# Kernel tuning notes

Hardware: AMD Instinct MI355X
Metric: run time of the kernel (lower is better)

The kernel has to match this reference:

```python
import jax, jax.numpy as jnp
import numpy as np
import math

BS, T = 256, 128
DD, DT, DB = 128, 16, 32
DH, NH, DS = 256, 4, 64
DHN = DH * NH


def _lin(key, din, dout):
    kw, kb = jax.random.split(key)
    w = jax.random.normal(kw, (din, dout), jnp.float32) * 0.02
    bb = jax.random.normal(kb, (dout,), jnp.float32) * 0.02
    return w, bb


def setup_inputs() -> dict:
    key = jax.random.key(0)
    ks = jax.random.split(key, 16)
    inp = {
        "x": jax.random.normal(ks[0], (BS, T, DD), jnp.float32),
        "a": jax.random.normal(ks[1], (BS, T, DT), jnp.float32),
        "m": jnp.ones((BS, T, DD), jnp.float32),
        "b": jax.random.normal(ks[2], (BS, DB), jnp.float32),
        "eps": jax.random.normal(ks[3], (T - 1, BS, DS), jnp.float32),
    }
    inp["bk_w"], inp["bk_b"] = _lin(ks[4], DD + DB, DH)
    inp["bv_w"], inp["bv_b"] = _lin(ks[5], DD + DB, DHN)
    inp["q_w"], inp["q_b"] = _lin(ks[6], DD + DT, DHN)
    inp["v_w"], inp["v_b"] = _lin(ks[7], DD + DT, DHN)
    inp["hk_w"], inp["hk_b"] = _lin(ks[8], DS, DH)
    inp["hv_w"], inp["hv_b"] = _lin(ks[9], DS, DHN)
    inp["mu1_w"], inp["mu1_b"] = _lin(ks[10], DHN, DS)
    inp["sg1_w"], inp["sg1_b"] = _lin(ks[11], DHN, DS)
    inp["mut_w"], inp["mut_b"] = _lin(ks[12], DHN, DS)
    inp["sgt_w"], inp["sgt_b"] = _lin(ks[13], DHN, DS)
    return inp


def reference(x, a, m, b, eps,
              bk_w, bk_b, bv_w, bv_b, q_w, q_b, v_w, v_b,
              hk_w, hk_b, hv_w, hv_b,
              mu1_w, mu1_b, sg1_w, sg1_b, mut_w, mut_b, sgt_w, sgt_b):
    bs = x.shape[0]
    inp = jnp.concatenate([x[:, 1:, :], a[:, :-1, :]], -1)   # [bs, T-1, DD+DT]
    mask = (jnp.sum(m[:, 1:, :], -1) > 0.0).astype(x.dtype)  # [bs, T-1]

    q_inp = jax.nn.relu(inp @ q_w + q_b).reshape(bs, -1, DH, NH)  # [bs,T-1,DH,NH]
    v_inp = (inp @ v_w + v_b).reshape(bs, -1, DH, NH)

    scale = 1.0 / math.sqrt(DH)

    def attn(key_vec):  # key_vec: [bs, DH]
        scores = jnp.einsum('bd,btdh->bth', key_vec, q_inp) * scale
        scores = jnp.where(mask[..., None] > 0, scores, -1e9)
        p = jax.nn.softmax(scores, axis=1)                 # over time
        return jnp.einsum('bth,btdh->bdh', p, v_inp).reshape(bs, DHN)

    xb = jnp.concatenate([x[:, 0, :], b], -1)              # [bs, DD+DB]
    key1 = jax.nn.relu(xb @ bk_w + bk_b)
    val1 = xb @ bv_w + bv_b
    h1 = jax.nn.relu(0.5 * (attn(key1) + val1))
    mu1 = h1 @ mu1_w + mu1_b
    sg1 = jax.nn.softplus(h1 @ sg1_w + sg1_b)
    z1 = mu1 + sg1 * eps[0]

    def step(z_prev, e):
        keyt = jax.nn.relu(z_prev @ hk_w + hk_b)
        valt = z_prev @ hv_w + hv_b
        ht = jax.nn.relu(0.5 * (attn(keyt) + valt))
        mu = ht @ mut_w + mut_b
        sg = jax.nn.softplus(ht @ sgt_w + sgt_b)
        z = mu + sg * e
        return z, (z, mu, sg)

    _, (zs, mus, sgs) = jax.lax.scan(step, z1, eps[1:])
    Z = jnp.moveaxis(jnp.concatenate([z1[None], zs], 0), 0, 1)    # [bs, T-1, DS]
    MU = jnp.moveaxis(jnp.concatenate([mu1[None], mus], 0), 0, 1)
    SG = jnp.moveaxis(jnp.concatenate([sg1[None], sgs], 0), 0, 1)
    return Z, MU, SG
```

## Files before the change

### kernel.cpp

```cpp
#include <hip/hip_runtime.h>
#include <hip/hip_bf16.h>
#include <stdint.h>

#define BS   256
#define T_   128
#define TP   127
#define DD   128
#define DT   16
#define DB   32
#define DH   256
#define NH   4
#define DS   64
#define DHN  1024

#define OFFV (256u*127u*64u)

typedef __attribute__((ext_vector_type(8))) short short8v;
typedef __attribute__((ext_vector_type(4))) float f32x4;
typedef __attribute__((ext_vector_type(2))) float f32x2;

__device__ __forceinline__ float bf16u(unsigned short u){ return __uint_as_float((unsigned)u << 16); }
__device__ __forceinline__ float bf16lo(unsigned u){ return __uint_as_float(u << 16); }
__device__ __forceinline__ float bf16hi(unsigned u){ return __uint_as_float(u & 0xffff0000u); }
__device__ __forceinline__ unsigned short f2bf(float f){
  unsigned u = __float_as_uint(f);
  u += 0x7fffu + ((u >> 16) & 1u);
  return (unsigned short)(u >> 16);
}
__device__ __forceinline__ unsigned pk2(float lo, float hi){
  return (unsigned)f2bf(lo) | ((unsigned)f2bf(hi) << 16);
}
__device__ __forceinline__ float softplus_f(float x){
  return fmaxf(x, 0.f) + log1pf(__expf(-fabsf(x)));
}
__device__ __forceinline__ unsigned pk4fp8(float f0, float f1, float f2, float f3){
  int pk8 = __builtin_amdgcn_cvt_pk_fp8_f32(f0, f1, 0, false);
  pk8     = __builtin_amdgcn_cvt_pk_fp8_f32(f2, f3, pk8, true);
  return (unsigned)pk8;
}

#define REP32(M) M(0) M(1) M(2) M(3) M(4) M(5) M(6) M(7) M(8) M(9) M(10) M(11) \
  M(12) M(13) M(14) M(15) M(16) M(17) M(18) M(19) M(20) M(21) M(22) M(23) \
  M(24) M(25) M(26) M(27) M(28) M(29) M(30) M(31)
#define REP8(M) M(0) M(1) M(2) M(3) M(4) M(5) M(6) M(7)

__global__ __launch_bounds__(256) void pack_w_kernel(
    const float* __restrict__ hk_w, const float* __restrict__ hv_w,
    const float* __restrict__ mut_w, const float* __restrict__ sgt_w,
    unsigned* __restrict__ hkp, unsigned* __restrict__ hvp,
    unsigned* __restrict__ mutp, unsigned* __restrict__ sgtp)
{
  int i = blockIdx.x * 256 + threadIdx.x;
  if (i < 32*256) { int s2 = i >> 8, d = i & 255;
    hkp[i] = pk2(hk_w[(2*s2)*256 + d], hk_w[(2*s2+1)*256 + d]); }
  if (i < 32*1024) { int s2 = i >> 10, j = i & 1023;
    hvp[i] = pk2(hv_w[(2*s2)*1024 + j], hv_w[(2*s2+1)*1024 + j]); }
  if (i < 512*64) { int J2 = i >> 6, k = i & 63;
    mutp[i] = pk2(mut_w[(2*J2)*64 + k], mut_w[(2*J2+1)*64 + k]);
    sgtp[i] = pk2(sgt_w[(2*J2)*64 + k], sgt_w[(2*J2+1)*64 + k]); }
}

#define LDA 168

__global__ __launch_bounds__(256) void proj_kernel(
    const float* __restrict__ x, const float* __restrict__ a,
    const float* __restrict__ q_w, const float* __restrict__ q_b,
    const float* __restrict__ v_w, const float* __restrict__ v_b,
    unsigned* __restrict__ Qf8, unsigned* __restrict__ Vf8)
{
  const int b    = blockIdx.x;
  const int tid  = threadIdx.x;
  const int lane = tid & 63;
  const int w    = tid >> 6;

  __shared__ __align__(16) unsigned short A_s[128 * LDA];
  __shared__ __align__(16) unsigned short BC_s[64 * LDA];

  for (int idx = tid; idx < 128 * DD; idx += 256) {
    int t = idx >> 7, k = idx & 127;
    float v = (t < TP) ? x[((size_t)b * T_ + 1 + t) * DD + k] : 0.f;
    A_s[t * LDA + k] = f2bf(v);
  }
  for (int idx = tid; idx < 128 * 40; idx += 256) {
    int t = idx / 40, kk = idx % 40;
    float v = (t < TP && kk < DT) ? a[((size_t)b * T_ + t) * DT + kk] : 0.f;
    A_s[t * LDA + 128 + kk] = f2bf(v);
  }
  __syncthreads();

  for (int nt = 0; nt < 32; ++nt) {
    const int n0 = nt * 64;
    const bool isQ = (n0 < DHN);
    const float* wsrc = isQ ? q_w : v_w;
    const float* bias = isQ ? q_b : v_b;
    const int nb = isQ ? n0 : (n0 - DHN);

    for (int idx = tid; idx < 160 * 64; idx += 256) {
      int k = idx >> 6, n = idx & 63;
      float v = (k < DD + DT) ? wsrc[(size_t)k * DHN + nb + n] : 0.f;
      BC_s[n * LDA + k] = f2bf(v);
    }
    __syncthreads();

    f32x4 acc[2][4];
#pragma unroll
    for (int mi = 0; mi < 2; ++mi)
#pragma unroll
      for (int ni = 0; ni < 4; ++ni) { f32x4 zz = {0.f,0.f,0.f,0.f}; acc[mi][ni] = zz; }
    const int mb = w * 32;
#pragma unroll
    for (int kc = 0; kc < 5; ++kc) {
      const int ko = kc * 32 + ((lane >> 4) << 3);
      short8v af[2], bf[4];
#pragma unroll
      for (int mi = 0; mi < 2; ++mi)
        af[mi] = *(const short8v*)&A_s[(mb + mi*16 + (lane & 15)) * LDA + ko];
#pragma unroll
      for (int ni = 0; ni < 4; ++ni)
        bf[ni] = *(const short8v*)&BC_s[(ni*16 + (lane & 15)) * LDA + ko];
#pragma unroll
      for (int mi = 0; mi < 2; ++mi)
#pragma unroll
        for (int ni = 0; ni < 4; ++ni)
          acc[mi][ni] = __builtin_amdgcn_mfma_f32_16x16x32_bf16(af[mi], bf[ni], acc[mi][ni], 0, 0, 0);
    }
    __syncthreads();

#pragma unroll
    for (int mi = 0; mi < 2; ++mi)
#pragma unroll
      for (int ni = 0; ni < 4; ++ni) {
        int cl = ni*16 + (lane & 15);
        float bb = bias[nb + cl];
#pragma unroll
        for (int q = 0; q < 4; ++q) {
          int t = mb + mi*16 + ((lane >> 4) << 2) + q;
          float vv = acc[mi][ni][q] + bb;
          if (isQ) vv = fmaxf(vv, 0.f);
          BC_s[t * 66 + cl] = f2bf(vv);
        }
      }
    __syncthreads();

    if (isQ) {
      for (int idx = tid; idx < 4 * 512; idx += 256) {
        int d4l = idx >> 9, r = idx & 511;
        int t = r >> 2, h = r & 3;
        const unsigned short* cr = &BC_s[t * 66 + d4l * 16 + h];
        unsigned pk = pk4fp8(bf16u(cr[0]), bf16u(cr[4]), bf16u(cr[8]), bf16u(cr[12]));
        Qf8[((size_t)b * 512 + r) * 64 + (n0 >> 4) + d4l] = pk;
      }
    } else {
      int c0v = n0 - DHN;
      for (int idx = tid; idx < 32 * 64; idx += 256) {
        int n = idx >> 6, jl = idx & 63;
        unsigned pk = pk4fp8(bf16u(BC_s[(4*n+0) * 66 + jl]), bf16u(BC_s[(4*n+1) * 66 + jl]),
                             bf16u(BC_s[(4*n+2) * 66 + jl]), bf16u(BC_s[(4*n+3) * 66 + jl]));
        Vf8[((size_t)b * 32 + n) * 1024 + c0v + jl] = pk;
      }
    }
    __syncthreads();
  }
}

__global__ __launch_bounds__(1024, 1)
void recur_kernel(
    const float* __restrict__ x, const float* __restrict__ bvec,
    const float* __restrict__ m, const float* __restrict__ eps,
    const float* __restrict__ bk_w, const float* __restrict__ bk_b,
    const float* __restrict__ bv_w, const float* __restrict__ bv_b,
    const float* __restrict__ hk_b, const float* __restrict__ hv_b,
    const float* __restrict__ mu1_w, const float* __restrict__ mu1_b,
    const float* __restrict__ sg1_w, const float* __restrict__ sg1_b,
    const float* __restrict__ mut_b, const float* __restrict__ sgt_b,
    const unsigned* __restrict__ hkp, const unsigned* __restrict__ hvp,
    const unsigned* __restrict__ mutp, const unsigned* __restrict__ sgtp,
    const unsigned* __restrict__ Qf8, const unsigned* __restrict__ Vf8,
    float* __restrict__ out)
{
  const int b    = blockIdx.x;
  const int tid  = threadIdx.x;
  const int lane = tid & 63;
  const int wvid = tid >> 6;

  extern __shared__ __align__(16) unsigned ldsV[];

  __shared__ __align__(16) float key_s[DH];
  __shared__ __align__(16) float sc[1024];
  __shared__ __align__(16) float p_T[4][128];
  __shared__ __align__(16) float ht_s[DHN];
  __shared__ __align__(16) float red[16 * 64];
  __shared__ __align__(16) float z_s[DS];
  __shared__ __align__(16) float xb[DD + DB];
  __shared__ float mask_s[128];
  __shared__ __align__(16) float hkb_s[DH];
  __shared__ __align__(16) float hvb_s[DHN];
  __shared__ float mtb_s[DS], stb_s[DS];

  if (tid < DD + DB) xb[tid] = (tid < DD) ? x[(size_t)b * T_ * DD + tid] : bvec[b * DB + (tid - DD)];
  if (tid >= 256 && tid < 512) hkb_s[tid - 256] = hk_b[tid - 256];
  hvb_s[tid] = hv_b[tid];
  if (tid < DS) { mtb_s[tid] = mut_b[tid]; stb_s[tid] = sgt_b[tid]; }
  if (tid < 512) ((float*)p_T)[tid] = 0.f;

  {
    const unsigned* vp = Vf8 + (size_t)b * 32 * 1024 + tid;
#pragma unroll
    for (int n = 0; n < 32; ++n) ldsV[n * 1024 + tid] = vp[n * 1024];
  }

  for (int t = wvid; t < TP; t += 16) {
    const float* mr = m + ((size_t)b * T_ + 1 + t) * DD;
    float s = mr[lane] + mr[lane + 64];
    for (int o = 1; o < 64; o <<= 1) s += __shfl_xor(s, o);
    if (lane == 0) mask_s[t] = (s > 0.f) ? 1.f : 0.f;
  }
  __syncthreads();

  const int r     = tid & 511;
  const int dhalf = tid >> 9;
  const int hW    = tid >> 8;
  const uint4* qrow = (const uint4*)(Qf8 + ((size_t)b * 512 + r) * 64 + dhalf * 32);
  const float* kb_base = &key_s[dhalf * 128];

  float myval = 0.f;

  for (int st = 0; st < TP; ++st) {
    if (st == 0) {
      float av = bv_b[tid];
      for (int s = 0; s < DD + DB; ++s) av = fmaf(xb[s], bv_w[(size_t)s * DHN + tid], av);
      myval = av;
      if (tid < 256) {
        float ak = bk_b[tid];
        for (int s = 0; s < DD + DB; ++s) ak = fmaf(xb[s], bk_w[s * DH + tid], ak);
        key_s[tid] = fmaxf(ak, 0.f);
      }
    } else {
      float av = hvb_s[tid];
#pragma unroll 8
      for (int s2 = 0; s2 < 32; ++s2) {
        float2 zz = *(const float2*)&z_s[s2 * 2];
        unsigned w0 = hvp[s2 * 1024 + tid];
        av = fmaf(zz.x, bf16lo(w0), av); av = fmaf(zz.y, bf16hi(w0), av);
      }
      myval = av;
      if (tid < 256) {
        float ak = hkb_s[tid];
#pragma unroll 8
        for (int s2 = 0; s2 < 32; ++s2) {
          float2 zz = *(const float2*)&z_s[s2 * 2];
          unsigned wq = hkp[s2 * 256 + tid];
          ak = fmaf(zz.x, bf16lo(wq), ak); ak = fmaf(zz.y, bf16hi(wq), ak);
        }
        key_s[tid] = fmaxf(ak, 0.f);
      }
    }
    __syncthreads();

    {
      float acc = 0.f;
#define SCD(wrd, koff) { f32x2 a01 = __builtin_amdgcn_cvt_pk_f32_fp8((wrd), false); \
      f32x2 a23 = __builtin_amdgcn_cvt_pk_f32_fp8((wrd), true); \
      float4 kk = *(const float4*)&kb_base[(koff)]; \
      acc = fmaf(a01.x, kk.x, acc); acc = fmaf(a01.y, kk.y, acc); \
      acc = fmaf(a23.x, kk.z, acc); acc = fmaf(a23.y, kk.w, acc); }
#define SCCH(c) { uint4 qc = qrow[c]; \
      SCD(qc.x, (c)*16 + 0) SCD(qc.y, (c)*16 + 4) SCD(qc.z, (c)*16 + 8) SCD(qc.w, (c)*16 + 12) }
      REP8(SCCH)
#undef SCCH
#undef SCD
      sc[tid] = acc;
    }
    __syncthreads();

    if (tid < 256) {
      int h = wvid, l = lane;
      int i1 = l * 4 + h;
      float v1 = (mask_s[l] > 0.f) ? (sc[i1] + sc[512 + i1]) * 0.0625f : -1e9f;
      float v2 = -3.0e38f;
      if (l + 64 < TP) {
        int i2 = (l + 64) * 4 + h;
        v2 = (mask_s[l + 64] > 0.f) ? (sc[i2] + sc[512 + i2]) * 0.0625f : -1e9f;
      }
      float mm = fmaxf(v1, v2);
      for (int o = 1; o < 64; o <<= 1) mm = fmaxf(mm, __shfl_xor(mm, o));
      float e1 = __expf(v1 - mm);
      float e2 = (l + 64 < TP) ? __expf(v2 - mm) : 0.f;
      float ssum = e1 + e2;
      for (int o = 1; o < 64; o <<= 1) ssum += __shfl_xor(ssum, o);
      float inv = 1.f / ssum;
      p_T[h][l] = e1 * inv;
      if (l + 64 < TP) p_T[h][l + 64] = e2 * inv;
    }
    __syncthreads();

    {
      float a = 0.f;
#define PVD(n) { unsigned wv8 = ldsV[(n) * 1024 + tid]; \
      float4 pp = *(const float4*)&p_T[hW][4 * (n)]; \
      f32x2 v01 = __builtin_amdgcn_cvt_pk_f32_fp8(wv8, false); \
      f32x2 v23 = __builtin_amdgcn_cvt_pk_f32_fp8(wv8, true); \
      a = fmaf(pp.x, v01.x, a); a = fmaf(pp.y, v01.y, a); \
      a = fmaf(pp.z, v23.x, a); a = fmaf(pp.w, v23.y, a); }
      REP32(PVD)
#undef PVD
      ht_s[tid] = fmaxf(0.5f * (a + myval), 0.f);
    }
    __syncthreads();

    {
      int k = tid & 63, sel = (tid >> 6) & 1, g = tid >> 7;
      float acc;
      if (st == 0) {
        const float* wsel = sel ? sg1_w : mu1_w;
        acc = 0.f;
        for (int jl = g * 128; jl < g * 128 + 128; ++jl)
          acc = fmaf(ht_s[jl], wsel[(size_t)jl * 64 + k], acc);
      } else {
        const unsigned* wp = sel ? sgtp : mutp;
        float a0 = 0.f, a1 = 0.f;
#pragma unroll 4
        for (int j2 = g * 64; j2 < g * 64 + 64; ++j2) {
          float2 hh = *(const float2*)&ht_s[j2 * 2];
          unsigned wm = wp[j2 * 64 + k];
          a0 = fmaf(hh.x, bf16lo(wm), a0);
          a1 = fmaf(hh.y, bf16hi(wm), a1);
        }
        acc = a0 + a1;
      }
      red[(sel * 8 + g) * 64 + k] = acc;
    }
    __syncthreads();

    if (tid < 64) {
      float mu = (st == 0) ? mu1_b[tid] : mtb_s[tid];
      float sl = (st == 0) ? sg1_b[tid] : stb_s[tid];
#pragma unroll
      for (int g = 0; g < 8; ++g) { mu += red[g * 64 + tid]; sl += red[(8 + g) * 64 + tid]; }
      float sg = softplus_f(sl);
      float z  = fmaf(sg, eps[((size_t)st * BS + b) * 64 + tid], mu);
      size_t o0 = ((size_t)b * TP + st) * 64 + tid;
      out[o0] = z; out[OFFV + o0] = mu; out[2ull * OFFV + o0] = sg;
      z_s[tid] = z;
    }
    __syncthreads();
  }
}

extern "C" void kernel_launch(void* const* d_in, const int* in_sizes, int n_in,
                              void* d_out, int out_size, void* d_ws, size_t ws_size,
                              hipStream_t stream) {
  const float* x    = (const float*)d_in[0];
  const float* a    = (const float*)d_in[1];
  const float* m    = (const float*)d_in[2];
  const float* bvec = (const float*)d_in[3];
  const float* eps  = (const float*)d_in[4];
  const float* bk_w = (const float*)d_in[5];
  const float* bk_b = (const float*)d_in[6];
  const float* bv_w = (const float*)d_in[7];
  const float* bv_b = (const float*)d_in[8];
  const float* q_w  = (const float*)d_in[9];
  const float* q_b  = (const float*)d_in[10];
  const float* v_w  = (const float*)d_in[11];
  const float* v_b  = (const float*)d_in[12];
  const float* hk_w = (const float*)d_in[13];
  const float* hk_b = (const float*)d_in[14];
  const float* hv_w = (const float*)d_in[15];
  const float* hv_b = (const float*)d_in[16];
  const float* mu1_w= (const float*)d_in[17];
  const float* mu1_b= (const float*)d_in[18];
  const float* sg1_w= (const float*)d_in[19];
  const float* sg1_b= (const float*)d_in[20];
  const float* mut_w= (const float*)d_in[21];
  const float* mut_b= (const float*)d_in[22];
  const float* sgt_w= (const float*)d_in[23];
  const float* sgt_b= (const float*)d_in[24];

  char* ws = (char*)d_ws;
  unsigned* Qf8  = (unsigned*)ws;
  unsigned* Vf8  = (unsigned*)(ws + (32ull << 20));
  unsigned* hkp  = (unsigned*)(ws + (64ull << 20));
  unsigned* hvp  = hkp + 32 * 256;
  unsigned* mutp = hvp + 32 * 1024;
  unsigned* sgtp = mutp + 512 * 64;

  pack_w_kernel<<<dim3(128), dim3(256), 0, stream>>>(hk_w, hv_w, mut_w, sgt_w,
                                                     hkp, hvp, mutp, sgtp);
  proj_kernel<<<dim3(256), dim3(256), 0, stream>>>(x, a, q_w, q_b, v_w, v_b, Qf8, Vf8);
  recur_kernel<<<dim3(256), dim3(1024), 131072, stream>>>(x, bvec, m, eps,
      bk_w, bk_b, bv_w, bv_b, hk_b, hv_b,
      mu1_w, mu1_b, sg1_w, sg1_b, mut_b, sgt_b,
      hkp, hvp, mutp, sgtp, Qf8, Vf8, (float*)d_out);
}
```

Baseline: 6.224 ms.

## Halve recurrence block to 512 threads, keep Q in registers, fp8 weights

```diff
diff --git a/kernel.cpp b/kernel.cpp
--- a/kernel.cpp
+++ b/kernel.cpp
@@ -20,16 +20,11 @@
 typedef __attribute__((ext_vector_type(2))) float f32x2;
 
 __device__ __forceinline__ float bf16u(unsigned short u){ return __uint_as_float((unsigned)u << 16); }
-__device__ __forceinline__ float bf16lo(unsigned u){ return __uint_as_float(u << 16); }
-__device__ __forceinline__ float bf16hi(unsigned u){ return __uint_as_float(u & 0xffff0000u); }
 __device__ __forceinline__ unsigned short f2bf(float f){
   unsigned u = __float_as_uint(f);
   u += 0x7fffu + ((u >> 16) & 1u);
   return (unsigned short)(u >> 16);
 }
-__device__ __forceinline__ unsigned pk2(float lo, float hi){
-  return (unsigned)f2bf(lo) | ((unsigned)f2bf(hi) << 16);
-}
 __device__ __forceinline__ float softplus_f(float x){
   return fmaxf(x, 0.f) + log1pf(__expf(-fabsf(x)));
 }
@@ -38,26 +33,29 @@
   pk8     = __builtin_amdgcn_cvt_pk_fp8_f32(f2, f3, pk8, true);
   return (unsigned)pk8;
 }
-
-#define REP32(M) M(0) M(1) M(2) M(3) M(4) M(5) M(6) M(7) M(8) M(9) M(10) M(11) \
-  M(12) M(13) M(14) M(15) M(16) M(17) M(18) M(19) M(20) M(21) M(22) M(23) \
-  M(24) M(25) M(26) M(27) M(28) M(29) M(30) M(31)
-#define REP8(M) M(0) M(1) M(2) M(3) M(4) M(5) M(6) M(7)
+#define CVT8(w, hi) __builtin_amdgcn_cvt_pk_f32_fp8((w), (hi))
+
+#define REP16(M) M(0) M(1) M(2) M(3) M(4) M(5) M(6) M(7) M(8) M(9) M(10) M(11) \
+  M(12) M(13) M(14) M(15)
 
 __global__ __launch_bounds__(256) void pack_w_kernel(
     const float* __restrict__ hk_w, const float* __restrict__ hv_w,
     const float* __restrict__ mut_w, const float* __restrict__ sgt_w,
-    unsigned* __restrict__ hkp, unsigned* __restrict__ hvp,
-    unsigned* __restrict__ mutp, unsigned* __restrict__ sgtp)
+    uint2* __restrict__ hvf, unsigned* __restrict__ hkf, unsigned* __restrict__ msf)
 {
   int i = blockIdx.x * 256 + threadIdx.x;
-  if (i < 32*256) { int s2 = i >> 8, d = i & 255;
-    hkp[i] = pk2(hk_w[(2*s2)*256 + d], hk_w[(2*s2+1)*256 + d]); }
-  if (i < 32*1024) { int s2 = i >> 10, j = i & 1023;
-    hvp[i] = pk2(hv_w[(2*s2)*1024 + j], hv_w[(2*s2+1)*1024 + j]); }
-  if (i < 512*64) { int J2 = i >> 6, k = i & 63;
-    mutp[i] = pk2(mut_w[(2*J2)*64 + k], mut_w[(2*J2+1)*64 + k]);
-    sgtp[i] = pk2(sgt_w[(2*J2)*64 + k], sgt_w[(2*J2+1)*64 + k]); }
+  if (i < 8192) { int s4 = i >> 9, j2 = i & 511;
+    const float* w0 = hv_w + (size_t)(4*s4)*1024 + 2*j2;
+    uint2 u;
+    u.x = pk4fp8(w0[0]*64.f, w0[1]*64.f, w0[1024]*64.f, w0[1025]*64.f);
+    u.y = pk4fp8(w0[2048]*64.f, w0[2049]*64.f, w0[3072]*64.f, w0[3073]*64.f);
+    hvf[i] = u; }
+  if (i < 4096) { int s4 = i >> 8, d = i & 255;
+    const float* w0 = hk_w + (size_t)(4*s4)*256 + d;
+    hkf[i] = pk4fp8(w0[0]*64.f, w0[256]*64.f, w0[512]*64.f, w0[768]*64.f); }
+  if (i < 32768) { int sel = i >> 14, j4 = (i >> 6) & 255, k = i & 63;
+    const float* w = (sel ? sgt_w : mut_w) + (size_t)(4*j4)*64 + k;
+    msf[i] = pk4fp8(w[0]*64.f, w[64]*64.f, w[128]*64.f, w[192]*64.f); }
 }
 
 #define LDA 168
@@ -66,7 +64,7 @@
     const float* __restrict__ x, const float* __restrict__ a,
     const float* __restrict__ q_w, const float* __restrict__ q_b,
     const float* __restrict__ v_w, const float* __restrict__ v_b,
-    unsigned* __restrict__ Qf8, unsigned* __restrict__ Vf8)
+    uint4* __restrict__ Qf8, unsigned* __restrict__ Vf8)
 {
   const int b    = blockIdx.x;
   const int tid  = threadIdx.x;
@@ -143,27 +141,32 @@
     __syncthreads();
 
     if (isQ) {
-      for (int idx = tid; idx < 4 * 512; idx += 256) {
-        int d4l = idx >> 9, r = idx & 511;
-        int t = r >> 2, h = r & 3;
-        const unsigned short* cr = &BC_s[t * 66 + d4l * 16 + h];
-        unsigned pk = pk4fp8(bf16u(cr[0]), bf16u(cr[4]), bf16u(cr[8]), bf16u(cr[12]));
-        Qf8[((size_t)b * 512 + r) * 64 + (n0 >> 4) + d4l] = pk;
+      int c = nt;
+      for (int idx = tid; idx < 512; idx += 256) {
+        int t = idx >> 2, h = idx & 3;
+        const unsigned short* base = &BC_s[t * 66 + h];
+        uint4 u;
+        u.x = pk4fp8(bf16u(base[ 0]), bf16u(base[ 4]), bf16u(base[ 8]), bf16u(base[12]));
+        u.y = pk4fp8(bf16u(base[16]), bf16u(base[20]), bf16u(base[24]), bf16u(base[28]));
+        u.z = pk4fp8(bf16u(base[32]), bf16u(base[36]), bf16u(base[40]), bf16u(base[44]));
+        u.w = pk4fp8(bf16u(base[48]), bf16u(base[52]), bf16u(base[56]), bf16u(base[60]));
+        Qf8[((size_t)b * 512 + idx) * 16 + c] = u;
       }
     } else {
-      int c0v = n0 - DHN;
-      for (int idx = tid; idx < 32 * 64; idx += 256) {
-        int n = idx >> 6, jl = idx & 63;
-        unsigned pk = pk4fp8(bf16u(BC_s[(4*n+0) * 66 + jl]), bf16u(BC_s[(4*n+1) * 66 + jl]),
-                             bf16u(BC_s[(4*n+2) * 66 + jl]), bf16u(BC_s[(4*n+3) * 66 + jl]));
-        Vf8[((size_t)b * 32 + n) * 1024 + c0v + jl] = pk;
-      }
-    }
-    __syncthreads();
-  }
-}
-
-__global__ __launch_bounds__(1024, 1)
+      int j2b = (n0 - DHN) >> 1;
+      for (int idx = tid; idx < 2048; idx += 256) {
+        int n = idx >> 6, rem = idx & 63, j2l = rem >> 1, d = rem & 1;
+        int cl = j2l * 2 + d;
+        unsigned pk = pk4fp8(bf16u(BC_s[(4*n+0)*66 + cl]), bf16u(BC_s[(4*n+1)*66 + cl]),
+                             bf16u(BC_s[(4*n+2)*66 + cl]), bf16u(BC_s[(4*n+3)*66 + cl]));
+        Vf8[(((size_t)b * 32 + n) * 512 + j2b + j2l) * 2 + d] = pk;
+      }
+    }
+    __syncthreads();
+  }
+}
+
+__global__ __launch_bounds__(512)
 void recur_kernel(
     const float* __restrict__ x, const float* __restrict__ bvec,
     const float* __restrict__ m, const float* __restrict__ eps,
@@ -173,9 +176,9 @@
     const float* __restrict__ mu1_w, const float* __restrict__ mu1_b,
     const float* __restrict__ sg1_w, const float* __restrict__ sg1_b,
     const float* __restrict__ mut_b, const float* __restrict__ sgt_b,
-    const unsigned* __restrict__ hkp, const unsigned* __restrict__ hvp,
-    const unsigned* __restrict__ mutp, const unsigned* __restrict__ sgtp,
-    const unsigned* __restrict__ Qf8, const unsigned* __restrict__ Vf8,
+    const uint2* __restrict__ hvf, const unsigned* __restrict__ hkf,
+    const unsigned* __restrict__ msf,
+    const uint4* __restrict__ Qf8, const uint2* __restrict__ Vf8,
     float* __restrict__ out)
 {
   const int b    = blockIdx.x;
@@ -183,13 +186,14 @@
   const int lane = tid & 63;
   const int wvid = tid >> 6;
 
-  extern __shared__ __align__(16) unsigned ldsV[];
+  extern __shared__ __align__(16) unsigned ldsRaw[];
+  uint2* ldsV = (uint2*)ldsRaw;
 
   __shared__ __align__(16) float key_s[DH];
-  __shared__ __align__(16) float sc[1024];
+  __shared__ __align__(16) float sc[512];
   __shared__ __align__(16) float p_T[4][128];
   __shared__ __align__(16) float ht_s[DHN];
-  __shared__ __align__(16) float red[16 * 64];
+  __shared__ __align__(16) float red[8 * 64];
   __shared__ __align__(16) float z_s[DS];
   __shared__ __align__(16) float xb[DD + DB];
   __shared__ float mask_s[128];
@@ -198,90 +202,97 @@
   __shared__ float mtb_s[DS], stb_s[DS];
 
   if (tid < DD + DB) xb[tid] = (tid < DD) ? x[(size_t)b * T_ * DD + tid] : bvec[b * DB + (tid - DD)];
-  if (tid >= 256 && tid < 512) hkb_s[tid - 256] = hk_b[tid - 256];
-  hvb_s[tid] = hv_b[tid];
+  if (tid >= 256) hkb_s[tid - 256] = hk_b[tid - 256];
+  hvb_s[tid] = hv_b[tid]; hvb_s[tid + 512] = hv_b[tid + 512];
   if (tid < DS) { mtb_s[tid] = mut_b[tid]; stb_s[tid] = sgt_b[tid]; }
-  if (tid < 512) ((float*)p_T)[tid] = 0.f;
-
-  {
-    const unsigned* vp = Vf8 + (size_t)b * 32 * 1024 + tid;
-#pragma unroll
-    for (int n = 0; n < 32; ++n) ldsV[n * 1024 + tid] = vp[n * 1024];
-  }
-
-  for (int t = wvid; t < TP; t += 16) {
+  ((float*)p_T)[tid] = 0.f;
+
+  for (int t = wvid; t < TP; t += 8) {
     const float* mr = m + ((size_t)b * T_ + 1 + t) * DD;
     float s = mr[lane] + mr[lane + 64];
     for (int o = 1; o < 64; o <<= 1) s += __shfl_xor(s, o);
     if (lane == 0) mask_s[t] = (s > 0.f) ? 1.f : 0.f;
   }
+  if (tid == 0) mask_s[127] = 0.f;
+
+  {
+    const uint2* vp = Vf8 + (size_t)b * 16384 + tid;
+#pragma unroll
+    for (int i = 0; i < 32; ++i) ldsV[i * 512 + tid] = vp[i * 512];
+  }
+
+  const uint4* qrow = Qf8 + ((size_t)b * 512 + tid) * 16;
+#define LDQ(c) uint4 qa##c = qrow[c];
+  REP16(LDQ)
+#undef LDQ
   __syncthreads();
 
-  const int r     = tid & 511;
-  const int dhalf = tid >> 9;
-  const int hW    = tid >> 8;
-  const uint4* qrow = (const uint4*)(Qf8 + ((size_t)b * 512 + r) * 64 + dhalf * 32);
-  const float* kb_base = &key_s[dhalf * 128];
-
-  float myval = 0.f;
+  const int hW = tid >> 7;
+  const float invs = 1.f / 64.f;
 
   for (int st = 0; st < TP; ++st) {
+    float myv0, myv1;
     if (st == 0) {
-      float av = bv_b[tid];
-      for (int s = 0; s < DD + DB; ++s) av = fmaf(xb[s], bv_w[(size_t)s * DHN + tid], av);
-      myval = av;
+      float a0 = bv_b[2*tid], a1 = bv_b[2*tid+1];
+      for (int s = 0; s < DD + DB; ++s) {
+        float xs = xb[s];
+        const float* rr = bv_w + (size_t)s * DHN + 2*tid;
+        a0 = fmaf(xs, rr[0], a0); a1 = fmaf(xs, rr[1], a1);
+      }
+      myv0 = a0; myv1 = a1;
       if (tid < 256) {
         float ak = bk_b[tid];
         for (int s = 0; s < DD + DB; ++s) ak = fmaf(xb[s], bk_w[s * DH + tid], ak);
         key_s[tid] = fmaxf(ak, 0.f);
       }
     } else {
-      float av = hvb_s[tid];
-#pragma unroll 8
-      for (int s2 = 0; s2 < 32; ++s2) {
-        float2 zz = *(const float2*)&z_s[s2 * 2];
-        unsigned w0 = hvp[s2 * 1024 + tid];
-        av = fmaf(zz.x, bf16lo(w0), av); av = fmaf(zz.y, bf16hi(w0), av);
-      }
-      myval = av;
+      float a0 = 0.f, a1 = 0.f;
+#pragma unroll
+      for (int s4 = 0; s4 < 16; ++s4) {
+        uint2 wv = hvf[s4 * 512 + tid];
+        float4 zz = *(const float4*)&z_s[s4 * 4];
+        f32x2 p0 = CVT8(wv.x, false), p1 = CVT8(wv.x, true);
+        f32x2 p2 = CVT8(wv.y, false), p3 = CVT8(wv.y, true);
+        a0 = fmaf(zz.x, p0.x, a0); a1 = fmaf(zz.x, p0.y, a1);
+        a0 = fmaf(zz.y, p1.x, a0); a1 = fmaf(zz.y, p1.y, a1);
+        a0 = fmaf(zz.z, p2.x, a0); a1 = fmaf(zz.z, p2.y, a1);
+        a0 = fmaf(zz.w, p3.x, a0); a1 = fmaf(zz.w, p3.y, a1);
+      }
+      myv0 = fmaf(a0, invs, hvb_s[2*tid]);
+      myv1 = fmaf(a1, invs, hvb_s[2*tid+1]);
       if (tid < 256) {
-        float ak = hkb_s[tid];
-#pragma unroll 8
-        for (int s2 = 0; s2 < 32; ++s2) {
-          float2 zz = *(const float2*)&z_s[s2 * 2];
-          unsigned wq = hkp[s2 * 256 + tid];
-          ak = fmaf(zz.x, bf16lo(wq), ak); ak = fmaf(zz.y, bf16hi(wq), ak);
+        float ak = 0.f;
+#pragma unroll
+        for (int s4 = 0; s4 < 16; ++s4) {
+          unsigned wq = hkf[s4 * 256 + tid];
+          float4 zz = *(const float4*)&z_s[s4 * 4];
+          f32x2 q0 = CVT8(wq, false), q1 = CVT8(wq, true);
+          ak = fmaf(zz.x, q0.x, ak); ak = fmaf(zz.y, q0.y, ak);
+          ak = fmaf(zz.z, q1.x, ak); ak = fmaf(zz.w, q1.y, ak);
         }
-        key_s[tid] = fmaxf(ak, 0.f);
+        key_s[tid] = fmaxf(fmaf(ak, invs, hkb_s[tid]), 0.f);
       }
     }
     __syncthreads();
 
     {
       float acc = 0.f;
-#define SCD(wrd, koff) { f32x2 a01 = __builtin_amdgcn_cvt_pk_f32_fp8((wrd), false); \
-      f32x2 a23 = __builtin_amdgcn_cvt_pk_f32_fp8((wrd), true); \
-      float4 kk = *(const float4*)&kb_base[(koff)]; \
-      acc = fmaf(a01.x, kk.x, acc); acc = fmaf(a01.y, kk.y, acc); \
-      acc = fmaf(a23.x, kk.z, acc); acc = fmaf(a23.y, kk.w, acc); }
-#define SCCH(c) { uint4 qc = qrow[c]; \
-      SCD(qc.x, (c)*16 + 0) SCD(qc.y, (c)*16 + 4) SCD(qc.z, (c)*16 + 8) SCD(qc.w, (c)*16 + 12) }
-      REP8(SCCH)
-#undef SCCH
+#define SCD(wrd, kidx) { f32x2 f01 = CVT8((wrd), false); f32x2 f23 = CVT8((wrd), true); \
+      float4 kk = *(const float4*)&key_s[(kidx) * 4]; \
+      acc = fmaf(f01.x, kk.x, acc); acc = fmaf(f01.y, kk.y, acc); \
+      acc = fmaf(f23.x, kk.z, acc); acc = fmaf(f23.y, kk.w, acc); }
+#define SCC(c) { SCD(qa##c.x, (c)*4+0) SCD(qa##c.y, (c)*4+1) SCD(qa##c.z, (c)*4+2) SCD(qa##c.w, (c)*4+3) }
+      REP16(SCC)
+#undef SCC
 #undef SCD
-      sc[tid] = acc;
+      sc[tid] = (mask_s[tid >> 2] > 0.f) ? acc * 0.0625f : -1e9f;
     }
     __syncthreads();
 
     if (tid < 256) {
       int h = wvid, l = lane;
-      int i1 = l * 4 + h;
-      float v1 = (mask_s[l] > 0.f) ? (sc[i1] + sc[512 + i1]) * 0.0625f : -1e9f;
-      float v2 = -3.0e38f;
-      if (l + 64 < TP) {
-        int i2 = (l + 64) * 4 + h;
-        v2 = (mask_s[l + 64] > 0.f) ? (sc[i2] + sc[512 + i2]) * 0.0625f : -1e9f;
-      }
+      float v1 = sc[l * 4 + h];
+      float v2 = (l + 64 < TP) ? sc[(l + 64) * 4 + h] : -3.0e38f;
       float mm = fmaxf(v1, v2);
       for (int o = 1; o < 64; o <<= 1) mm = fmaxf(mm, __shfl_xor(mm, o));
       float e1 = __expf(v1 - mm);
@@ -295,48 +306,53 @@
     __syncthreads();
 
     {
-      float a = 0.f;
-#define PVD(n) { unsigned wv8 = ldsV[(n) * 1024 + tid]; \
-      float4 pp = *(const float4*)&p_T[hW][4 * (n)]; \
-      f32x2 v01 = __builtin_amdgcn_cvt_pk_f32_fp8(wv8, false); \
-      f32x2 v23 = __builtin_amdgcn_cvt_pk_f32_fp8(wv8, true); \
-      a = fmaf(pp.x, v01.x, a); a = fmaf(pp.y, v01.y, a); \
-      a = fmaf(pp.z, v23.x, a); a = fmaf(pp.w, v23.y, a); }
-      REP32(PVD)
-#undef PVD
-      ht_s[tid] = fmaxf(0.5f * (a + myval), 0.f);
+      float a0 = 0.f, a1 = 0.f;
+#pragma unroll
+      for (int n = 0; n < 32; ++n) {
+        uint2 vv = ldsV[n * 512 + tid];
+        float4 pp = *(const float4*)&p_T[hW][4 * n];
+        f32x2 v0 = CVT8(vv.x, false), v1 = CVT8(vv.x, true);
+        f32x2 w0 = CVT8(vv.y, false), w1 = CVT8(vv.y, true);
+        a0 = fmaf(pp.x, v0.x, a0); a0 = fmaf(pp.y, v0.y, a0);
+        a0 = fmaf(pp.z, v1.x, a0); a0 = fmaf(pp.w, v1.y, a0);
+        a1 = fmaf(pp.x, w0.x, a1); a1 = fmaf(pp.y, w0.y, a1);
+        a1 = fmaf(pp.z, w1.x, a1); a1 = fmaf(pp.w, w1.y, a1);
+      }
+      float2 hh;
+      hh.x = fmaxf(0.5f * (a0 + myv0), 0.f);
+      hh.y = fmaxf(0.5f * (a1 + myv1), 0.f);
+      *(float2*)&ht_s[2 * tid] = hh;
     }
     __syncthreads();
 
     {
       int k = tid & 63, sel = (tid >> 6) & 1, g = tid >> 7;
-      float acc;
+      float acc = 0.f;
       if (st == 0) {
         const float* wsel = sel ? sg1_w : mu1_w;
-        acc = 0.f;
-        for (int jl = g * 128; jl < g * 128 + 128; ++jl)
+        for (int jl = g * 256; jl < g * 256 + 256; ++jl)
           acc = fmaf(ht_s[jl], wsel[(size_t)jl * 64 + k], acc);
       } else {
-        const unsigned* wp = sel ? sgtp : mutp;
-        float a0 = 0.f, a1 = 0.f;
-#pragma unroll 4
-        for (int j2 = g * 64; j2 < g * 64 + 64; ++j2) {
-          float2 hh = *(const float2*)&ht_s[j2 * 2];
-          unsigned wm = wp[j2 * 64 + k];
-          a0 = fmaf(hh.x, bf16lo(wm), a0);
-          a1 = fmaf(hh.y, bf16hi(wm), a1);
+        const unsigned* wp = msf + sel * 16384;
+#pragma unroll 8
+        for (int j4 = g * 64; j4 < g * 64 + 64; ++j4) {
+          unsigned wm = wp[j4 * 64 + k];
+          float4 hh = *(const float4*)&ht_s[j4 * 4];
+          f32x2 f0 = CVT8(wm, false), f1 = CVT8(wm, true);
+          acc = fmaf(hh.x, f0.x, acc); acc = fmaf(hh.y, f0.y, acc);
+          acc = fmaf(hh.z, f1.x, acc); acc = fmaf(hh.w, f1.y, acc);
         }
-        acc = a0 + a1;
-      }
-      red[(sel * 8 + g) * 64 + k] = acc;
+      }
+      red[(sel * 4 + g) * 64 + k] = acc;
     }
     __syncthreads();
 
     if (tid < 64) {
-      float mu = (st == 0) ? mu1_b[tid] : mtb_s[tid];
-      float sl = (st == 0) ? sg1_b[tid] : stb_s[tid];
-#pragma unroll
-      for (int g = 0; g < 8; ++g) { mu += red[g * 64 + tid]; sl += red[(8 + g) * 64 + tid]; }
+      float wsc = (st == 0) ? 1.f : invs;
+      float mu = ((st == 0) ? mu1_b[tid] : mtb_s[tid])
+               + (red[tid] + red[64 + tid] + red[128 + tid] + red[192 + tid]) * wsc;
+      float sl = ((st == 0) ? sg1_b[tid] : stb_s[tid])
+               + (red[256 + tid] + red[320 + tid] + red[384 + tid] + red[448 + tid]) * wsc;
       float sg = softplus_f(sl);
       float z  = fmaf(sg, eps[((size_t)st * BS + b) * 64 + tid], mu);
       size_t o0 = ((size_t)b * TP + st) * 64 + tid;
@@ -377,18 +393,18 @@
   const float* sgt_b= (const float*)d_in[24];
 
   char* ws = (char*)d_ws;
-  unsigned* Qf8  = (unsigned*)ws;
-  unsigned* Vf8  = (unsigned*)(ws + (32ull << 20));
-  unsigned* hkp  = (unsigned*)(ws + (64ull << 20));
-  unsigned* hvp  = hkp + 32 * 256;
-  unsigned* mutp = hvp + 32 * 1024;
-  unsigned* sgtp = mutp + 512 * 64;
+  uint4*    Qf8 = (uint4*)ws;
+  unsigned* Vf8 = (unsigned*)(ws + (32ull << 20));
+  uint2*    hvf = (uint2*)(ws + (64ull << 20));
+  unsigned* hkf = (unsigned*)(ws + (64ull << 20) + (64u << 10));
+  unsigned* msf = (unsigned*)(ws + (64ull << 20) + (80u << 10));
 
   pack_w_kernel<<<dim3(128), dim3(256), 0, stream>>>(hk_w, hv_w, mut_w, sgt_w,
-                                                     hkp, hvp, mutp, sgtp);
-  proj_kernel<<<dim3(256), dim3(256), 0, stream>>>(x, a, q_w, q_b, v_w, v_b, Qf8, Vf8);
-  recur_kernel<<<dim3(256), dim3(1024), 131072, stream>>>(x, bvec, m, eps,
+                                                     hvf, hkf, msf);
+  proj_kernel<<<dim3(256), dim3(256), 0, stream>>>(x, a, q_w, q_b, v_w, v_b,
+                                                   Qf8, Vf8);
+  recur_kernel<<<dim3(256), dim3(512), 131072, stream>>>(x, bvec, m, eps,
       bk_w, bk_b, bv_w, bv_b, hk_b, hv_b,
       mu1_w, mu1_b, sg1_w, sg1_b, mut_b, sgt_b,
-      hkp, hvp, mutp, sgtp, Qf8, Vf8, (float*)d_out);
-}
+      hvf, hkf, msf, Qf8, (const uint2*)Vf8, (float*)d_out);
+}
```

Measured after the change: 6.447 ms. +3.6%, slower.
